# Optimization experiments

Measured on AMD Instinct MI355X. Metric: run time of the kernel, lower is better.

Reference implementation:

```python
import jax, jax.numpy as jnp
import numpy as np

B, H, W = 8, 128, 128
ITERS = 1000


def _face_conductivities(k):
    # arithmetic-mean face conductivities with edge replication at the boundary
    kp = jnp.pad(k, ((0, 0), (1, 1), (1, 1)), mode='edge')
    c = kp[:, 1:-1, 1:-1]
    kN = 0.5 * (c + kp[:, :-2, 1:-1])
    kS = 0.5 * (c + kp[:, 2:, 1:-1])
    kW = 0.5 * (c + kp[:, 1:-1, :-2])
    kE = 0.5 * (c + kp[:, 1:-1, 2:])
    return kN, kS, kW, kE


def gauss_solver(conductivity, iterations):
    """Jacobi-style relaxation of steady diffusion div(k grad T)=0.
    Dirichlet BC: T=1 at top row, T=0 at bottom row; zero-flux (edge
    replication) on the left/right sides. Vectorized over batch."""
    kN, kS, kW, kE = _face_conductivities(conductivity)
    denom = kN + kS + kW + kE  # precomputed outside the iteration loop
    T0 = jnp.zeros_like(conductivity).at[:, 0, :].set(1.0)

    def step(T, _):
        Tp = jnp.pad(T, ((0, 0), (1, 1), (1, 1)), mode='edge')
        Tn = (kN * Tp[:, :-2, 1:-1] + kS * Tp[:, 2:, 1:-1]
              + kW * Tp[:, 1:-1, :-2] + kE * Tp[:, 1:-1, 2:]) / denom
        # re-impose Dirichlet boundary rows
        Tn = Tn.at[:, 0, :].set(1.0).at[:, -1, :].set(0.0)
        return Tn, None

    T, _ = jax.lax.scan(step, T0, None, length=iterations)
    return T


def flux_kappa(conductivity, Ts):
    # Jy = -k * dT/dy, padded back to full grid; kappa = total flux across mid row
    Jy = -conductivity[:, :-1, :] * (Ts[:, 1:, :] - Ts[:, :-1, :]) / 1.0
    Jy = jnp.pad(Jy, ((0, 0), (0, 1), (0, 0)), mode='constant', constant_values=0)
    kappas = jnp.sum(Jy[:, conductivity.shape[1] // 2, :], axis=-1)
    return kappas


def setup_inputs() -> dict:
    key = jax.random.key(0)
    # strictly positive conductivity field in [0.1, 1.0)
    u = jax.random.uniform(key, (B, H, W), dtype=jnp.float32)
    conductivity = 0.1 + 0.9 * u
    return {"conductivity": conductivity, "iterations": ITERS}


def reference(conductivity, iterations):
    T = gauss_solver(conductivity, iterations)
    return flux_kappa(conductivity, T)
```

## Files before the change

kernel.cpp:

```cpp
#include <hip/hip_runtime.h>


#define GH 128
#define GW 128
#define NW 16
#define RPW 8
#define NT 1024

typedef float v2f __attribute__((ext_vector_type(2)));

__device__ __forceinline__ float dpp_shr1(float old_v, float src) {
    return __int_as_float(__builtin_amdgcn_update_dpp(
        __float_as_int(old_v), __float_as_int(src), 0x138, 0xf, 0xf, false));
}
__device__ __forceinline__ float dpp_shl1(float old_v, float src) {
    return __int_as_float(__builtin_amdgcn_update_dpp(
        __float_as_int(old_v), __float_as_int(src), 0x130, 0xf, 0xf, false));
}

__global__ void __launch_bounds__(NT)
jacobi_flux_kernel(const float* __restrict__ k_all,
                   const int* __restrict__ iters_p,
                   float* __restrict__ out)
{
    __shared__ __align__(16) v2f sTop[2][NW][64];
    __shared__ __align__(16) v2f sBot[2][NW][64];

    const int b   = blockIdx.x;
    const int tid = threadIdx.x;
    const int l   = tid & 63;
    const int w   = tid >> 6;
    const int R0  = w * RPW;
    const int c0  = l * 2;
    const float* kb = k_all + b * GH * GW;
    const int iters = *iters_p;

    const int wUp = (w == 0)      ? 0      : w - 1;
    const int wDn = (w == NW - 1) ? NW - 1 : w + 1;
    const bool gTop = (w == 0);
    const bool gBot = (w == NW - 1);

    v2f rN[RPW], rS[RPW], cM[RPW], cLR[RPW];
    #pragma unroll
    for (int i = 0; i < RPW; ++i) {
        const int r  = R0 + i;
        const int ru = (r == 0)      ? 0      : r - 1;
        const int rd = (r == GH - 1) ? GH - 1 : r + 1;
        float v[2][4];
        #pragma unroll
        for (int jj = 0; jj < 2; ++jj) {
            const int c  = c0 + jj;
            const int cl = (c == 0)      ? 0      : c - 1;
            const int cr = (c == GW - 1) ? GW - 1 : c + 1;
            float kc = kb[r * GW + c];
            float kn = 0.5f * (kc + kb[ru * GW + c]);
            float ks = 0.5f * (kc + kb[rd * GW + c]);
            float kw = 0.5f * (kc + kb[r * GW + cl]);
            float ke = 0.5f * (kc + kb[r * GW + cr]);
            float inv = 1.0f / (kn + ks + kw + ke);
            v[jj][0] = kn * inv; v[jj][1] = ks * inv;
            v[jj][2] = kw * inv; v[jj][3] = ke * inv;
        }
        rN[i]  = (v2f){v[0][0], v[1][0]};
        rS[i]  = (v2f){v[0][1], v[1][1]};
        cM[i]  = (v2f){v[0][3], v[1][2]};
        cLR[i] = (v2f){v[0][2], v[1][3]};
    }

    v2f A[RPW], B[RPW];
    #pragma unroll
    for (int i = 0; i < RPW; ++i)
        A[i] = (R0 + i == 0) ? (v2f){1.0f, 1.0f} : (v2f){0.0f, 0.0f};

    sTop[0][w][l] = A[0];
    sBot[0][w][l] = A[RPW - 1];
    __syncthreads();

    auto step = [&](const v2f (&src)[RPW], v2f (&dst)[RPW], int rp, int wp) {
        v2f hu = sBot[rp][wUp][l];
        v2f hd = sTop[rp][wDn][l];

        #pragma unroll
        for (int i = 0; i < RPW; ++i) {
            v2f cc = src[i];
            v2f s;
            s.x = dpp_shr1(cc.x, cc.y);
            s.y = dpp_shl1(cc.y, cc.x);
            v2f up = (i == 0)       ? hu : src[i - 1];
            v2f dn = (i == RPW - 1) ? hd : src[i + 1];
            dst[i] = __builtin_elementwise_fma(rN[i], up,
                     __builtin_elementwise_fma(rS[i], dn,
                     __builtin_elementwise_fma(cLR[i], s, cM[i] * cc.yx)));
        }
        if (gTop) dst[0]       = (v2f){1.0f, 1.0f};
        if (gBot) dst[RPW - 1] = (v2f){0.0f, 0.0f};

        sTop[wp][w][l] = dst[0];
        sBot[wp][w][l] = dst[RPW - 1];
        __syncthreads();
    };

    const int nPairs = iters >> 1;
    for (int it = 0; it < nPairs; ++it) {
        step(A, B, 0, 1);
        step(B, A, 1, 0);
    }
    if (iters & 1) {
        step(A, B, 0, 1);
        #pragma unroll
        for (int i = 0; i < RPW; ++i) A[i] = B[i];
    }

    if (w == 8) {
        float partial = kb[64 * GW + c0]     * (A[1].x - A[0].x)
                      + kb[64 * GW + c0 + 1] * (A[1].y - A[0].y);
        #pragma unroll
        for (int off = 32; off > 0; off >>= 1)
            partial += __shfl_down(partial, off, 64);
        if (l == 0) out[b] = -partial;
    }
}

extern "C" void kernel_launch(void* const* d_in, const int* in_sizes, int n_in,
                              void* d_out, int out_size, void* d_ws, size_t ws_size,
                              hipStream_t stream)
{
    const float* k     = (const float*)d_in[0];
    const int*   iters = (const int*)d_in[1];
    float*       out   = (float*)d_out;
    jacobi_flux_kernel<<<dim3(8), dim3(NT), 0, stream>>>(k, iters, out);
}
```

Baseline: 589.4 us.

## Split each batch grid across two blocks with global-memory seam exchange

Each batch image is now split across two workgroups of 64 rows each, giving 16 blocks instead of 8 and halving the rows per wave. The two halves swap their seam rows every iteration through a double-buffered workspace, using release/acquire flag spinning at agent scope. Each seam wave computes its boundary row first, so the remaining rows can overlap the exchange. The cost is a cross-workgroup global-memory round trip every iteration, which may reach across XCDs. The flags are also never reset between launches, so correctness depends on the workspace being zeroed on each call.

```diff
diff --git a/kernel.cpp b/kernel.cpp
--- a/kernel.cpp
+++ b/kernel.cpp
@@ -4,7 +4,7 @@
 #define GH 128
 #define GW 128
 #define NW 16
-#define RPW 8
+#define RPW 4
 #define NT 1024
 
 typedef float v2f __attribute__((ext_vector_type(2)));
@@ -21,24 +21,35 @@
 __global__ void __launch_bounds__(NT)
 jacobi_flux_kernel(const float* __restrict__ k_all,
                    const int* __restrict__ iters_p,
-                   float* __restrict__ out)
+                   float* __restrict__ out,
+                   float* __restrict__ ws)
 {
     __shared__ __align__(16) v2f sTop[2][NW][64];
     __shared__ __align__(16) v2f sBot[2][NW][64];
 
-    const int b   = blockIdx.x;
+    const int b   = blockIdx.x & 7;
+    const int h   = blockIdx.x >> 3;
     const int tid = threadIdx.x;
     const int l   = tid & 63;
     const int w   = tid >> 6;
-    const int R0  = w * RPW;
+    const int R0  = h * 64 + w * RPW;
     const int c0  = l * 2;
     const float* kb = k_all + b * GH * GW;
     const int iters = *iters_p;
 
+    float*       myBuf = ws + b * 512 + h * 256;
+    const float* nbBuf = ws + b * 512 + (1 - h) * 256;
+    int* flags  = (int*)(ws + 8 * 512);
+    int* myFlag = flags + b * 32 + h * 16;
+    int* nbFlag = flags + b * 32 + (1 - h) * 16;
+    const bool seamDn = (h == 0 && w == NW - 1);
+    const bool seamUp = (h == 1 && w == 0);
+    const bool isSeam = seamDn || seamUp;
+
     const int wUp = (w == 0)      ? 0      : w - 1;
     const int wDn = (w == NW - 1) ? NW - 1 : w + 1;
-    const bool gTop = (w == 0);
-    const bool gBot = (w == NW - 1);
+    const bool gTop = (h == 0 && w == 0);
+    const bool gBot = (h == 1 && w == NW - 1);
 
     v2f rN[RPW], rS[RPW], cM[RPW], cLR[RPW];
     #pragma unroll
@@ -76,22 +87,56 @@
     sBot[0][w][l] = A[RPW - 1];
     __syncthreads();
 
-    auto step = [&](const v2f (&src)[RPW], v2f (&dst)[RPW], int rp, int wp) {
+    auto applyRow = [&](const v2f (&src)[RPW], v2f (&dst)[RPW],
+                        int i, v2f up, v2f dn) {
+        v2f cc = src[i];
+        v2f s;
+        s.x = dpp_shr1(cc.x, cc.y);
+        s.y = dpp_shl1(cc.y, cc.x);
+        dst[i] = __builtin_elementwise_fma(rN[i], up,
+                 __builtin_elementwise_fma(rS[i], dn,
+                 __builtin_elementwise_fma(cLR[i], s, cM[i] * cc.yx)));
+    };
+
+    auto step = [&](const v2f (&src)[RPW], v2f (&dst)[RPW],
+                    int rp, int wp, int it) {
         v2f hu = sBot[rp][wUp][l];
         v2f hd = sTop[rp][wDn][l];
 
-        #pragma unroll
-        for (int i = 0; i < RPW; ++i) {
-            v2f cc = src[i];
-            v2f s;
-            s.x = dpp_shr1(cc.x, cc.y);
-            s.y = dpp_shl1(cc.y, cc.x);
-            v2f up = (i == 0)       ? hu : src[i - 1];
-            v2f dn = (i == RPW - 1) ? hd : src[i + 1];
-            dst[i] = __builtin_elementwise_fma(rN[i], up,
-                     __builtin_elementwise_fma(rS[i], dn,
-                     __builtin_elementwise_fma(cLR[i], s, cM[i] * cc.yx)));
+        if (isSeam) {
+            v2f ext = (v2f){0.0f, 0.0f};
+            if (it > 0) {
+                while (__hip_atomic_load(nbFlag, __ATOMIC_RELAXED,
+                                         __HIP_MEMORY_SCOPE_AGENT) < it) {}
+                __builtin_amdgcn_fence(__ATOMIC_ACQUIRE, "agent");
+                ext = *(const v2f*)(nbBuf + (it & 1) * GW + c0);
+            }
+            if (seamDn) applyRow(src, dst, RPW - 1, src[RPW - 2], ext);
+            else        applyRow(src, dst, 0,       ext,          src[1]);
+            const int sr = seamDn ? (RPW - 1) : 0;
+            *(v2f*)(myBuf + ((it + 1) & 1) * GW + c0) = dst[sr];
+            if (l == 0)
+                __hip_atomic_store(myFlag, it + 1, __ATOMIC_RELEASE,
+                                   __HIP_MEMORY_SCOPE_AGENT);
+            if (seamDn) {
+                applyRow(src, dst, 0, hu, src[1]);
+                #pragma unroll
+                for (int i = 1; i < RPW - 1; ++i)
+                    applyRow(src, dst, i, src[i - 1], src[i + 1]);
+            } else {
+                #pragma unroll
+                for (int i = 1; i < RPW - 1; ++i)
+                    applyRow(src, dst, i, src[i - 1], src[i + 1]);
+                applyRow(src, dst, RPW - 1, src[RPW - 2], hd);
+            }
+        } else {
+            applyRow(src, dst, 0, hu, src[1]);
+            #pragma unroll
+            for (int i = 1; i < RPW - 1; ++i)
+                applyRow(src, dst, i, src[i - 1], src[i + 1]);
+            applyRow(src, dst, RPW - 1, src[RPW - 2], hd);
         }
+
         if (gTop) dst[0]       = (v2f){1.0f, 1.0f};
         if (gBot) dst[RPW - 1] = (v2f){0.0f, 0.0f};
 
@@ -100,18 +145,19 @@
         __syncthreads();
     };
 
+    int it = 0;
     const int nPairs = iters >> 1;
-    for (int it = 0; it < nPairs; ++it) {
-        step(A, B, 0, 1);
-        step(B, A, 1, 0);
+    for (int s = 0; s < nPairs; ++s) {
+        step(A, B, 0, 1, it); ++it;
+        step(B, A, 1, 0, it); ++it;
     }
     if (iters & 1) {
-        step(A, B, 0, 1);
+        step(A, B, 0, 1, it);
         #pragma unroll
         for (int i = 0; i < RPW; ++i) A[i] = B[i];
     }
 
-    if (w == 8) {
+    if (h == 1 && w == 0) {
         float partial = kb[64 * GW + c0]     * (A[1].x - A[0].x)
                       + kb[64 * GW + c0 + 1] * (A[1].y - A[0].y);
         #pragma unroll
@@ -128,5 +174,6 @@
     const float* k     = (const float*)d_in[0];
     const int*   iters = (const int*)d_in[1];
     float*       out   = (float*)d_out;
-    jacobi_flux_kernel<<<dim3(8), dim3(NT), 0, stream>>>(k, iters, out);
+    float*       ws    = (float*)d_ws;
+    jacobi_flux_kernel<<<dim3(16), dim3(NT), 0, stream>>>(k, iters, out, ws);
 }
```

Result: slower. 2.009 ms (+240.9%).
